# Kernel optimization log

Measured on AMD Instinct MI355X. Metric: run time of the kernel, lower is better.

## Reference

```python
import jax, jax.numpy as jnp
import numpy as np

EPS = 1e-5
PDIM, QKD, DIM = 64, 16, 256
SCALE = QKD ** -0.5


def setup_inputs() -> dict:
    key = jax.random.key(0)
    ks = jax.random.split(key, 13)
    B, H, W = 8, 64, 64
    return {
        "x": jax.random.normal(ks[0], (B, DIM, H, W), jnp.float32),
        "gn_g": jax.random.uniform(ks[1], (PDIM,), jnp.float32, 0.5, 1.5),
        "gn_b": jax.random.normal(ks[2], (PDIM,), jnp.float32) * 0.1,
        "qkv_w": jax.random.normal(ks[3], (2 * QKD + PDIM, PDIM), jnp.float32) * (PDIM ** -0.5),
        "qkv_bn_g": jax.random.uniform(ks[4], (2 * QKD + PDIM,), jnp.float32, 0.5, 1.5),
        "qkv_bn_b": jax.random.normal(ks[5], (2 * QKD + PDIM,), jnp.float32) * 0.1,
        "qkv_rm": jax.random.normal(ks[6], (2 * QKD + PDIM,), jnp.float32) * 0.1,
        "qkv_rv": jax.random.uniform(ks[7], (2 * QKD + PDIM,), jnp.float32, 0.5, 1.5),
        "proj_w": jax.random.normal(ks[8], (DIM, DIM), jnp.float32) * (DIM ** -0.5),
        "proj_bn_g": jax.random.uniform(ks[9], (DIM,), jnp.float32, 0.5, 1.5),
        "proj_bn_b": jax.random.normal(ks[10], (DIM,), jnp.float32) * 0.1,
        "proj_rm": jax.random.normal(ks[11], (DIM,), jnp.float32) * 0.1,
        "proj_rv": jax.random.uniform(ks[12], (DIM,), jnp.float32, 0.5, 1.5),
    }


def _bn(y, g, b, rm, rv):
    # inference BatchNorm over channel axis 1 of [B,C,H,W]
    inv = g / jnp.sqrt(rv + EPS)
    return y * inv[None, :, None, None] + (b - rm * inv)[None, :, None, None]


def reference(x, gn_g, gn_b, qkv_w, qkv_bn_g, qkv_bn_b, qkv_rm, qkv_rv,
              proj_w, proj_bn_g, proj_bn_b, proj_rm, proj_rv):
    B, C, H, W = x.shape
    x1, x2 = x[:, :PDIM], x[:, PDIM:]
    # GroupNorm with 1 group: normalize over (C,H,W) per sample
    mu = jnp.mean(x1, axis=(1, 2, 3), keepdims=True)
    var = jnp.var(x1, axis=(1, 2, 3), keepdims=True)
    x1n = (x1 - mu) / jnp.sqrt(var + EPS)
    x1n = x1n * gn_g[None, :, None, None] + gn_b[None, :, None, None]
    # qkv: 1x1 conv + BN
    qkv = jnp.einsum('bchw,oc->bohw', x1n, qkv_w)
    qkv = _bn(qkv, qkv_bn_g, qkv_bn_b, qkv_rm, qkv_rv)
    q, k, v = qkv[:, :QKD], qkv[:, QKD:2 * QKD], qkv[:, 2 * QKD:]
    N = H * W
    q = q.reshape(B, QKD, N)
    k = k.reshape(B, QKD, N)
    v = v.reshape(B, PDIM, N)
    attn = jnp.einsum('bcn,bcm->bnm', q, k) * SCALE  # [B,N,N]
    attn = jax.nn.softmax(attn, axis=-1)
    x1_attn = jnp.einsum('bcm,bnm->bcn', v, attn).reshape(B, PDIM, H, W)
    xc = jnp.concatenate([x1_attn, x2], axis=1)
    # proj: ReLU -> 1x1 conv -> BN
    y = jnp.einsum('bchw,oc->bohw', jax.nn.relu(xc), proj_w)
    return _bn(y, proj_bn_g, proj_bn_b, proj_rm, proj_rv)
```

## Files before the change

kernel.cpp:

```cpp
#include <hip/hip_runtime.h>
#include <hip/hip_bf16.h>

typedef __bf16 bf16;
typedef __bf16 bf16x4 __attribute__((ext_vector_type(4)));
typedef __bf16 bf16x8 __attribute__((ext_vector_type(8)));
typedef float  f32x16 __attribute__((ext_vector_type(16)));

#define MFMA32 __builtin_amdgcn_mfma_f32_32x32x16_bf16
#define EPSV 1e-5f
#define QSCALE 0.36067376022224085f

__device__ __forceinline__ f32x16 fzero16() {
  f32x16 z;
#pragma unroll
  for (int i = 0; i < 16; ++i) z[i] = 0.f;
  return z;
}

__global__ __launch_bounds__(256) void k_stats_partial(const float* __restrict__ x,
                                                       float* __restrict__ part) {
  const int b = blockIdx.x >> 5, k = blockIdx.x & 31;
  const float* p = x + (size_t)b * 256 * 4096 + k * 8192;
  const int t = threadIdx.x;
  float s = 0.f, q = 0.f;
#pragma unroll
  for (int j = 0; j < 8; ++j) {
    float4 v = ((const float4*)p)[t + j * 256];
    s += v.x + v.y + v.z + v.w;
    q += v.x * v.x + v.y * v.y + v.z * v.z + v.w * v.w;
  }
  __shared__ float ls[256], lq[256];
  ls[t] = s; lq[t] = q;
  __syncthreads();
  for (int off = 128; off > 0; off >>= 1) {
    if (t < off) { ls[t] += ls[t + off]; lq[t] += lq[t + off]; }
    __syncthreads();
  }
  if (t == 0) { part[blockIdx.x * 2] = ls[0]; part[blockIdx.x * 2 + 1] = lq[0]; }
}

__global__ __launch_bounds__(256) void k_stats_final(const float* __restrict__ part,
                                                     float* __restrict__ stats) {
  const int t = threadIdx.x, b = t >> 5, k = t & 31;
  float s = part[(b * 32 + k) * 2], q = part[(b * 32 + k) * 2 + 1];
  for (int off = 16; off > 0; off >>= 1) {
    s += __shfl_down(s, off, 32);
    q += __shfl_down(q, off, 32);
  }
  if (k == 0) {
    const float inv_n = 1.f / 262144.f;
    const float mu = s * inv_n;
    const float var = q * inv_n - mu * mu;
    stats[b * 2] = mu;
    stats[b * 2 + 1] = rsqrtf(var + EPSV);
  }
}

__global__ __launch_bounds__(256) void k_qkv(
    const float* __restrict__ x, const float* __restrict__ gn_g, const float* __restrict__ gn_b,
    const float* __restrict__ qkv_w, const float* __restrict__ bn_g, const float* __restrict__ bn_b,
    const float* __restrict__ bn_rm, const float* __restrict__ bn_rv,
    const float* __restrict__ stats,
    bf16* __restrict__ qw, bf16* __restrict__ kw, bf16* __restrict__ vw) {
  const int b = blockIdx.x >> 6, tile = blockIdx.x & 63;
  const int n0 = tile * 64, t = threadIdx.x;
  __shared__ float xn[64][68];
  __shared__ float W[64][96];
  __shared__ float beta_s[96];
  const float mu = stats[b * 2], rstd = stats[b * 2 + 1];
  {
    const int c = t >> 2, f = t & 3;
    const float A = rstd * gn_g[c], B = gn_b[c] - mu * A;
    const float* xr = x + ((size_t)b * 256 + c) * 4096 + n0;
#pragma unroll
    for (int j = 0; j < 4; ++j) {
      float4 v = ((const float4*)xr)[f * 4 + j];
      const int nb = f * 16 + j * 4;
      xn[c][nb + 0] = v.x * A + B; xn[c][nb + 1] = v.y * A + B;
      xn[c][nb + 2] = v.z * A + B; xn[c][nb + 3] = v.w * A + B;
    }
  }
  for (int oc = t; oc < 96 * 8; oc += 256) {
    const int o = oc >> 3, ch = (oc & 7) * 8;
    const float inv = bn_g[o] * rsqrtf(bn_rv[o] + EPSV);
    if (ch == 0) beta_s[o] = bn_b[o] - bn_rm[o] * inv;
    const float* wr = qkv_w + o * 64 + ch;
#pragma unroll
    for (int i = 0; i < 8; ++i) W[ch + i][o] = wr[i] * inv;
  }
  __syncthreads();
  const int o_l = t & 31, ng = t >> 5;
#pragma unroll 1
  for (int p = 0; p < 3; ++p) {
    const int o = p * 32 + o_l;
    float acc[8];
#pragma unroll
    for (int j = 0; j < 8; ++j) acc[j] = 0.f;
    for (int c = 0; c < 64; ++c) {
      const float wv = W[c][o];
      const float* xr = &xn[c][ng * 8];
#pragma unroll
      for (int j = 0; j < 8; ++j) acc[j] += wv * xr[j];
    }
    const float beta = beta_s[o];
    const int nb = n0 + ng * 8;
    if (p == 0) {
      if (o < 16) {
#pragma unroll
        for (int j = 0; j < 8; ++j)
          qw[((size_t)b * 4096 + nb + j) * 16 + o] = (bf16)((acc[j] + beta) * QSCALE);
      } else {
#pragma unroll
        for (int j = 0; j < 8; ++j)
          kw[((size_t)b * 4096 + nb + j) * 16 + (o - 16)] = (bf16)(acc[j] + beta);
      }
    } else {
      const int c = (p - 1) * 32 + o_l;
      const int IT = nb >> 5;
      const int m4 = nb & 31;
      const int f  = ((m4 >> 4) << 1) + (c >> 5);
      const int b3 = (m4 >> 3) & 1;
      char* base = (char*)vw + (size_t)b * 524288 + (size_t)IT * 4096 +
                   f * 1024 + (c & 31) * 16 + b3 * 8;
      bf16x4 pk0, pk1;
#pragma unroll
      for (int i = 0; i < 4; ++i) {
        pk0[i] = (bf16)(acc[i] + beta);
        pk1[i] = (bf16)(acc[4 + i] + beta);
      }
      *(bf16x4*)base = pk0;
      *(bf16x4*)(base + 512) = pk1;
    }
  }
}

__global__ __launch_bounds__(512, 4) void k_attn(
    const bf16* __restrict__ qw, const bf16* __restrict__ kw,
    const bf16* __restrict__ vw, const float* __restrict__ x,
    bf16* __restrict__ xc) {
  __shared__ __align__(16) char smem[33792];
  const int orig = blockIdx.x;
  const int wg = (orig & 7) * 64 + (orig >> 3);
  const int b = wg >> 6, qblk = wg & 63;
  const int t = threadIdx.x;
  const int wid = t >> 6, l = t & 63, ln = l & 31, g = l >> 5;
  const int qsub = wid & 1, kr = wid >> 1;
  const int m0 = kr * 1024;

  const bf16* qb = qw + (size_t)b * 4096 * 16;
  const char* kb = (const char*)(kw + (size_t)b * 4096 * 16);
  const char* vfb = (const char*)vw + (size_t)b * 524288;

  const char* kptr = kb + (size_t)(m0 + ln) * 32 + 16 * g;
  const char* vptr = vfb + (size_t)(m0 >> 5) * 4096 + l * 16;

  const int nq = qblk * 64 + qsub * 32 + ln;
  const bf16x8 qf = *(const bf16x8*)(qb + (size_t)nq * 16 + g * 8);

  f32x16 O0 = fzero16(), O1 = fzero16();
  float l_run = 0.f;

#pragma unroll 1
  for (int it = 0; it < 32; ++it) {
    const uint4 kc  = *(const uint4*)(kptr + it * 1024);
    const uint4 va0 = *(const uint4*)(vptr + it * 4096);
    const uint4 vb0 = *(const uint4*)(vptr + it * 4096 + 1024);
    const uint4 va1 = *(const uint4*)(vptr + it * 4096 + 2048);
    const uint4 vb1 = *(const uint4*)(vptr + it * 4096 + 3072);
    f32x16 S = MFMA32(__builtin_bit_cast(bf16x8, kc), qf, fzero16(), 0, 0, 0);
    float ts = 0.f;
#pragma unroll
    for (int r = 0; r < 16; ++r) { S[r] = __builtin_amdgcn_exp2f(S[r]); ts += S[r]; }
    ts += __shfl_xor(ts, 32, 64);
    l_run += ts;
    bf16x8 pb0, pb1;
#pragma unroll
    for (int r = 0; r < 8; ++r) { pb0[r] = (bf16)S[r]; pb1[r] = (bf16)S[r + 8]; }
    O0 = MFMA32(__builtin_bit_cast(bf16x8, va0), pb0, O0, 0, 0, 0);
    O1 = MFMA32(__builtin_bit_cast(bf16x8, vb0), pb0, O1, 0, 0, 0);
    O0 = MFMA32(__builtin_bit_cast(bf16x8, va1), pb1, O0, 0, 0, 0);
    O1 = MFMA32(__builtin_bit_cast(bf16x8, vb1), pb1, O1, 0, 0, 0);
  }

  {
    char* orow = smem + wid * 4096 + ln * 128;
    const int msk = 2 * (ln & 7);
#pragma unroll
    for (int h = 0; h < 2; ++h) {
      const f32x16& O = h ? O1 : O0;
#pragma unroll
      for (int j = 0; j < 4; ++j) {
        bf16x4 e;
#pragma unroll
        for (int i = 0; i < 4; ++i) e[i] = (bf16)O[4 * j + i];
        const int chunk = h * 8 + 2 * j + g;
        *(bf16x4*)(orow + ((chunk ^ msk) << 3)) = e;
      }
    }
    if (g == 0) *(float*)(smem + 32768 + wid * 128 + ln * 4) = l_run;
  }
  __syncthreads();

  {
    const int qs = t >> 8, tt = t & 255;
    const int n = tt >> 3, k8 = tt & 7;
    float L = 0.f;
    float acc[8];
#pragma unroll
    for (int e = 0; e < 8; ++e) acc[e] = 0.f;
#pragma unroll
    for (int kr_ = 0; kr_ < 4; ++kr_) {
      const int wsrc = kr_ * 2 + qs;
      L += *(const float*)(smem + 32768 + wsrc * 128 + n * 4);
      const bf16x8 v = *(const bf16x8*)(smem + wsrc * 4096 + n * 128 +
                                        (((2 * k8) ^ (2 * (n & 7))) << 3));
#pragma unroll
      for (int e = 0; e < 8; ++e) acc[e] += (float)v[e];
    }
    const float rL = 1.0f / L;
    bf16x8 o8;
#pragma unroll
    for (int e = 0; e < 8; ++e) o8[e] = (bf16)fmaxf(acc[e] * rL, 0.f);
    *(bf16x8*)(xc + ((size_t)b * 4096 + qblk * 64 + qs * 32 + n) * 256 + k8 * 8) = o8;
  }
  __syncthreads();

  {
    unsigned* tile_u = (unsigned*)smem;
    const float* xb = x + ((size_t)b * 256 + 64) * 4096 + qblk * 64;
#pragma unroll
    for (int i = 0; i < 3; ++i) {
      const int idx = i * 512 + t;
      const int cp = idx >> 4, f = idx & 15;
      const float4 a = *(const float4*)(xb + (size_t)(2 * cp) * 4096 + f * 4);
      const float4 c4 = *(const float4*)(xb + (size_t)(2 * cp + 1) * 4096 + f * 4);
      const float av[4] = {a.x, a.y, a.z, a.w};
      const float cv[4] = {c4.x, c4.y, c4.z, c4.w};
#pragma unroll
      for (int e = 0; e < 4; ++e) {
        const unsigned u =
            (unsigned)__builtin_bit_cast(unsigned short, (bf16)fmaxf(av[e], 0.f)) |
            ((unsigned)__builtin_bit_cast(unsigned short, (bf16)fmaxf(cv[e], 0.f)) << 16);
        tile_u[(f * 4 + e) * 97 + cp] = u;
      }
    }
    __syncthreads();
#pragma unroll
    for (int i = 0; i < 3; ++i) {
      const int idx = i * 512 + t;
      const int n = idx / 24, q = idx % 24;
      const uint4 d = *(const uint4*)&tile_u[n * 97 + q * 4];
      *(uint4*)(xc + ((size_t)b * 4096 + qblk * 64 + n) * 256 + 64 + q * 8) = d;
    }
  }
}

__global__ __launch_bounds__(256, 2) void k_proj(
    const bf16* __restrict__ xc, const float* __restrict__ pw,
    const float* __restrict__ bn_g, const float* __restrict__ bn_b,
    const float* __restrict__ bn_rm, const float* __restrict__ bn_rv,
    float* __restrict__ out) {
  const int orig = blockIdx.x;
  const int wg = (orig & 7) * 64 + (orig >> 3);
  const int b = wg >> 6, rem = wg & 63, nt = rem >> 1, oh = rem & 1;
  const int n0 = nt * 128, o0 = oh * 128;
  const int t = threadIdx.x, w = t >> 6, l = t & 63, ln = l & 31, g = l >> 5;

  __shared__ __align__(16) bf16 pws[128 * 256];
  __shared__ float beta_s[128];

  {
    const int o = t >> 1, half = t & 1;
    const float inv = bn_g[o0 + o] * rsqrtf(bn_rv[o0 + o] + EPSV);
    if (half == 0) beta_s[o] = bn_b[o0 + o] - bn_rm[o0 + o] * inv;
    const float* wr = pw + (size_t)(o0 + o) * 256 + half * 128;
    const int s_hh = (o & 15) * 8;
#pragma unroll
    for (int j = 0; j < 16; ++j) {
      const float4 a = ((const float4*)wr)[j * 2];
      const float4 c4 = ((const float4*)wr)[j * 2 + 1];
      bf16x8 v8;
      v8[0] = (bf16)(a.x * inv);  v8[1] = (bf16)(a.y * inv);
      v8[2] = (bf16)(a.z * inv);  v8[3] = (bf16)(a.w * inv);
      v8[4] = (bf16)(c4.x * inv); v8[5] = (bf16)(c4.y * inv);
      v8[6] = (bf16)(c4.z * inv); v8[7] = (bf16)(c4.w * inv);
      *(bf16x8*)&pws[o * 256 + ((half * 128 + j * 8) ^ s_hh)] = v8;
    }
  }
  __syncthreads();

  const bf16* xrow = xc + ((size_t)b * 4096 + n0 + w * 32 + ln) * 256;
  const int sw = (ln & 15) * 8;
  f32x16 acc0 = fzero16(), acc1 = fzero16(), acc2 = fzero16(), acc3 = fzero16();
#pragma unroll 4
  for (int ck = 0; ck < 256; ck += 16) {
    const bf16x8 bfrag = *(const bf16x8*)(xrow + ck + g * 8);
    const int cidx = (ck + g * 8) ^ sw;
    const bf16x8 a0 = *(const bf16x8*)&pws[(ln) * 256 + cidx];
    const bf16x8 a1 = *(const bf16x8*)&pws[(32 + ln) * 256 + cidx];
    const bf16x8 a2 = *(const bf16x8*)&pws[(64 + ln) * 256 + cidx];
    const bf16x8 a3 = *(const bf16x8*)&pws[(96 + ln) * 256 + cidx];
    acc0 = MFMA32(a0, bfrag, acc0, 0, 0, 0);
    acc1 = MFMA32(a1, bfrag, acc1, 0, 0, 0);
    acc2 = MFMA32(a2, bfrag, acc2, 0, 0, 0);
    acc3 = MFMA32(a3, bfrag, acc3, 0, 0, 0);
  }
  const int ncol = n0 + w * 32 + ln;
  float* ob = out + (size_t)b * 256 * 4096 + ncol;
#pragma unroll
  for (int og = 0; og < 4; ++og) {
    const f32x16& A = og == 0 ? acc0 : og == 1 ? acc1 : og == 2 ? acc2 : acc3;
#pragma unroll
    for (int r = 0; r < 16; ++r) {
      const int o_loc = og * 32 + (r & 3) + 8 * (r >> 2) + 4 * g;
      ob[(size_t)(o0 + o_loc) * 4096] = A[r] + beta_s[o_loc];
    }
  }
}

extern "C" void kernel_launch(void* const* d_in, const int* in_sizes, int n_in,
                              void* d_out, int out_size, void* d_ws, size_t ws_size,
                              hipStream_t stream) {
  (void)in_sizes; (void)n_in; (void)out_size; (void)ws_size;
  const float* x        = (const float*)d_in[0];
  const float* gn_g     = (const float*)d_in[1];
  const float* gn_b     = (const float*)d_in[2];
  const float* qkv_w    = (const float*)d_in[3];
  const float* qkv_bn_g = (const float*)d_in[4];
  const float* qkv_bn_b = (const float*)d_in[5];
  const float* qkv_rm   = (const float*)d_in[6];
  const float* qkv_rv   = (const float*)d_in[7];
  const float* proj_w   = (const float*)d_in[8];
  const float* proj_bn_g = (const float*)d_in[9];
  const float* proj_bn_b = (const float*)d_in[10];
  const float* proj_rm  = (const float*)d_in[11];
  const float* proj_rv  = (const float*)d_in[12];

  char* ws = (char*)d_ws;
  float* part  = (float*)ws;
  float* stats = (float*)(ws + 4096);
  bf16* qw = (bf16*)(ws + 8192);
  bf16* kw = (bf16*)(ws + 8192 + (1u << 20));
  bf16* vw = (bf16*)(ws + 8192 + (2u << 20));
  bf16* xc = (bf16*)(ws + 8192 + (6u << 20));

  k_stats_partial<<<256, 256, 0, stream>>>(x, part);
  k_stats_final<<<1, 256, 0, stream>>>(part, stats);
  k_qkv<<<512, 256, 0, stream>>>(x, gn_g, gn_b, qkv_w, qkv_bn_g, qkv_bn_b,
                                 qkv_rm, qkv_rv, stats, qw, kw, vw);
  k_attn<<<512, 512, 0, stream>>>(qw, kw, vw, x, xc);
  k_proj<<<512, 256, 0, stream>>>(xc, proj_w, proj_bn_g, proj_bn_b,
                                  proj_rm, proj_rv, (float*)d_out);
}
```

Baseline: 90.46 us.

## Split attention work into 1024 blocks of 32 queries with 8-way key split

Each attention workgroup now handles 32 queries instead of 64, with all eight waves splitting the keys eight ways (512 keys each) rather than four ways across two query sub-blocks. The grid doubles to 1024 blocks, launch bounds ask for 8 blocks per CU, and the K fragment load is software-prefetched one iteration ahead. The goal is more parallelism and better latency hiding on the MI355X CUs. In exchange, every query now pays an 8-way cross-wave reduction, Q/K/V is read twice as often in total, and the x2 copy epilogue leaves some threads idle.

```diff
diff --git a/kernel.cpp b/kernel.cpp
--- a/kernel.cpp
+++ b/kernel.cpp
@@ -134,18 +134,17 @@
   }
 }
 
-__global__ __launch_bounds__(512, 4) void k_attn(
+__global__ __launch_bounds__(512, 8) void k_attn(
     const bf16* __restrict__ qw, const bf16* __restrict__ kw,
     const bf16* __restrict__ vw, const float* __restrict__ x,
     bf16* __restrict__ xc) {
   __shared__ __align__(16) char smem[33792];
   const int orig = blockIdx.x;
-  const int wg = (orig & 7) * 64 + (orig >> 3);
-  const int b = wg >> 6, qblk = wg & 63;
+  const int wg = (orig & 7) * 128 + (orig >> 3);
+  const int b = wg >> 7, qblk = wg & 127;
   const int t = threadIdx.x;
   const int wid = t >> 6, l = t & 63, ln = l & 31, g = l >> 5;
-  const int qsub = wid & 1, kr = wid >> 1;
-  const int m0 = kr * 1024;
+  const int m0 = wid * 512;
 
   const bf16* qb = qw + (size_t)b * 4096 * 16;
   const char* kb = (const char*)(kw + (size_t)b * 4096 * 16);
@@ -154,20 +153,22 @@
   const char* kptr = kb + (size_t)(m0 + ln) * 32 + 16 * g;
   const char* vptr = vfb + (size_t)(m0 >> 5) * 4096 + l * 16;
 
-  const int nq = qblk * 64 + qsub * 32 + ln;
+  const int nq = qblk * 32 + ln;
   const bf16x8 qf = *(const bf16x8*)(qb + (size_t)nq * 16 + g * 8);
 
   f32x16 O0 = fzero16(), O1 = fzero16();
   float l_run = 0.f;
 
+  uint4 kc = *(const uint4*)kptr;
 #pragma unroll 1
-  for (int it = 0; it < 32; ++it) {
-    const uint4 kc  = *(const uint4*)(kptr + it * 1024);
+  for (int it = 0; it < 16; ++it) {
     const uint4 va0 = *(const uint4*)(vptr + it * 4096);
     const uint4 vb0 = *(const uint4*)(vptr + it * 4096 + 1024);
     const uint4 va1 = *(const uint4*)(vptr + it * 4096 + 2048);
     const uint4 vb1 = *(const uint4*)(vptr + it * 4096 + 3072);
-    f32x16 S = MFMA32(__builtin_bit_cast(bf16x8, kc), qf, fzero16(), 0, 0, 0);
+    const uint4 kcur = kc;
+    if (it + 1 < 16) kc = *(const uint4*)(kptr + (it + 1) * 1024);
+    f32x16 S = MFMA32(__builtin_bit_cast(bf16x8, kcur), qf, fzero16(), 0, 0, 0);
     float ts = 0.f;
 #pragma unroll
     for (int r = 0; r < 16; ++r) { S[r] = __builtin_amdgcn_exp2f(S[r]); ts += S[r]; }
@@ -202,55 +203,57 @@
   __syncthreads();
 
   {
-    const int qs = t >> 8, tt = t & 255;
-    const int n = tt >> 3, k8 = tt & 7;
+    const int n = t >> 4, chunk = t & 15;
+    const int off = ((chunk ^ (2 * (n & 7))) << 3);
     float L = 0.f;
-    float acc[8];
-#pragma unroll
-    for (int e = 0; e < 8; ++e) acc[e] = 0.f;
-#pragma unroll
-    for (int kr_ = 0; kr_ < 4; ++kr_) {
-      const int wsrc = kr_ * 2 + qs;
-      L += *(const float*)(smem + 32768 + wsrc * 128 + n * 4);
-      const bf16x8 v = *(const bf16x8*)(smem + wsrc * 4096 + n * 128 +
-                                        (((2 * k8) ^ (2 * (n & 7))) << 3));
-#pragma unroll
-      for (int e = 0; e < 8; ++e) acc[e] += (float)v[e];
+    float acc[4];
+#pragma unroll
+    for (int e = 0; e < 4; ++e) acc[e] = 0.f;
+#pragma unroll
+    for (int w_ = 0; w_ < 8; ++w_) {
+      L += *(const float*)(smem + 32768 + w_ * 128 + n * 4);
+      const bf16x4 v = *(const bf16x4*)(smem + w_ * 4096 + n * 128 + off);
+#pragma unroll
+      for (int e = 0; e < 4; ++e) acc[e] += (float)v[e];
     }
     const float rL = 1.0f / L;
-    bf16x8 o8;
-#pragma unroll
-    for (int e = 0; e < 8; ++e) o8[e] = (bf16)fmaxf(acc[e] * rL, 0.f);
-    *(bf16x8*)(xc + ((size_t)b * 4096 + qblk * 64 + qs * 32 + n) * 256 + k8 * 8) = o8;
+    bf16x4 o4;
+#pragma unroll
+    for (int e = 0; e < 4; ++e) o4[e] = (bf16)fmaxf(acc[e] * rL, 0.f);
+    *(bf16x4*)(xc + ((size_t)b * 4096 + qblk * 32 + n) * 256 + chunk * 4) = o4;
   }
   __syncthreads();
 
   {
     unsigned* tile_u = (unsigned*)smem;
-    const float* xb = x + ((size_t)b * 256 + 64) * 4096 + qblk * 64;
-#pragma unroll
-    for (int i = 0; i < 3; ++i) {
+    const float* xb = x + ((size_t)b * 256 + 64) * 4096 + qblk * 32;
+#pragma unroll
+    for (int i = 0; i < 2; ++i) {
       const int idx = i * 512 + t;
-      const int cp = idx >> 4, f = idx & 15;
-      const float4 a = *(const float4*)(xb + (size_t)(2 * cp) * 4096 + f * 4);
-      const float4 c4 = *(const float4*)(xb + (size_t)(2 * cp + 1) * 4096 + f * 4);
-      const float av[4] = {a.x, a.y, a.z, a.w};
-      const float cv[4] = {c4.x, c4.y, c4.z, c4.w};
-#pragma unroll
-      for (int e = 0; e < 4; ++e) {
-        const unsigned u =
-            (unsigned)__builtin_bit_cast(unsigned short, (bf16)fmaxf(av[e], 0.f)) |
-            ((unsigned)__builtin_bit_cast(unsigned short, (bf16)fmaxf(cv[e], 0.f)) << 16);
-        tile_u[(f * 4 + e) * 97 + cp] = u;
+      if (idx < 768) {
+        const int cp = idx >> 3, f = idx & 7;
+        const float4 a = *(const float4*)(xb + (size_t)(2 * cp) * 4096 + f * 4);
+        const float4 c4 = *(const float4*)(xb + (size_t)(2 * cp + 1) * 4096 + f * 4);
+        const float av[4] = {a.x, a.y, a.z, a.w};
+        const float cv[4] = {c4.x, c4.y, c4.z, c4.w};
+#pragma unroll
+        for (int e = 0; e < 4; ++e) {
+          const unsigned u =
+              (unsigned)__builtin_bit_cast(unsigned short, (bf16)fmaxf(av[e], 0.f)) |
+              ((unsigned)__builtin_bit_cast(unsigned short, (bf16)fmaxf(cv[e], 0.f)) << 16);
+          tile_u[(f * 4 + e) * 97 + cp] = u;
+        }
       }
     }
     __syncthreads();
 #pragma unroll
-    for (int i = 0; i < 3; ++i) {
+    for (int i = 0; i < 2; ++i) {
       const int idx = i * 512 + t;
-      const int n = idx / 24, q = idx % 24;
-      const uint4 d = *(const uint4*)&tile_u[n * 97 + q * 4];
-      *(uint4*)(xc + ((size_t)b * 4096 + qblk * 64 + n) * 256 + 64 + q * 8) = d;
+      if (idx < 768) {
+        const int n = idx / 24, q = idx % 24;
+        const uint4 d = *(const uint4*)&tile_u[n * 97 + q * 4];
+        *(uint4*)(xc + ((size_t)b * 4096 + qblk * 32 + n) * 256 + 64 + q * 8) = d;
+      }
     }
   }
 }
@@ -348,7 +351,7 @@
   k_stats_final<<<1, 256, 0, stream>>>(part, stats);
   k_qkv<<<512, 256, 0, stream>>>(x, gn_g, gn_b, qkv_w, qkv_bn_g, qkv_bn_b,
                                  qkv_rm, qkv_rv, stats, qw, kw, vw);
-  k_attn<<<512, 512, 0, stream>>>(qw, kw, vw, x, xc);
+  k_attn<<<1024, 512, 0, stream>>>(qw, kw, vw, x, xc);
   k_proj<<<512, 256, 0, stream>>>(xc, proj_w, proj_bn_g, proj_bn_b,
                                   proj_rm, proj_rv, (float*)d_out);
 }
```

Measured after the change: 192.4 us. 113% more time.
